# Performance work log

Hardware: AMD Instinct MI355X
Metric: run time of the kernel (lower is better)

## Reference

```python
import jax, jax.numpy as jnp
import numpy as np

DIM = 2048
HEADS = 16
HEAD_DIM = DIM // HEADS  # 128
FF = 8192
MAX_SEQ = 4096
B, S, PREV = 2, 2048, 1024
EPS = 1e-6
ROTARY_BASE = 10000.0


def setup_inputs() -> dict:
    key = jax.random.key(0)
    ks = jax.random.split(key, 16)
    n = lambda k, shape: jax.random.normal(k, shape, jnp.float32) * 0.02
    inp = {
        "x": jax.random.normal(ks[0], (B, S, DIM), jnp.float32),
        "k_cache": jax.random.normal(ks[1], (B, HEADS, PREV, HEAD_DIM), jnp.float32),
        "v_cache": jax.random.normal(ks[2], (B, HEADS, PREV, HEAD_DIM), jnp.float32),
        "attn_norm_w": jnp.ones((DIM,), jnp.float32),
        "ffn_norm_w": jnp.ones((DIM,), jnp.float32),
        "wq": n(ks[3], (DIM, DIM)), "bq": jnp.zeros((DIM,), jnp.float32),
        "wk": n(ks[4], (DIM, DIM)), "bk": jnp.zeros((DIM,), jnp.float32),
        "wv": n(ks[5], (DIM, DIM)), "bv": jnp.zeros((DIM,), jnp.float32),
        "wo": n(ks[6], (DIM, DIM)), "bo": jnp.zeros((DIM,), jnp.float32),
        "w_gate": n(ks[7], (DIM, FF)), "b_gate": jnp.zeros((FF,), jnp.float32),
        "w_val": n(ks[8], (DIM, FF)), "b_val": jnp.zeros((FF,), jnp.float32),
        "w_proj": n(ks[9], (FF, DIM)), "b_proj": jnp.zeros((DIM,), jnp.float32),
    }
    # precompute_freqs_cis as (cos, sin) pair: [MAX_SEQ, HEAD_DIM//2]
    freqs = 1.0 / (ROTARY_BASE ** (np.arange(0, HEAD_DIM, 2)[: HEAD_DIM // 2].astype(np.float32) / HEAD_DIM))
    ang = np.outer(np.arange(MAX_SEQ), freqs).astype(np.float32)
    inp["freqs_cos"] = jnp.asarray(np.cos(ang))
    inp["freqs_sin"] = jnp.asarray(np.sin(ang))
    inp["start_pos"] = PREV
    inp["cache_limit"] = 4096
    return inp


def rmsnorm(x, w):
    return x * jax.lax.rsqrt(jnp.mean(x * x, axis=-1, keepdims=True) + EPS) * w


def rope(x, cos, sin):
    # x: [B, H, S, D]; cos/sin: [1, 1, S, D/2] (complex multiply on even/odd pairs)
    xp = x.reshape(*x.shape[:-1], HEAD_DIM // 2, 2)
    x0, x1 = xp[..., 0], xp[..., 1]
    return jnp.stack([x0 * cos - x1 * sin, x0 * sin + x1 * cos], axis=-1).reshape(x.shape)


def reference(x, k_cache, v_cache, attn_norm_w, ffn_norm_w, wq, bq, wk, bk, wv, bv,
              wo, bo, w_gate, b_gate, w_val, b_val, w_proj, b_proj,
              freqs_cos, freqs_sin, start_pos, cache_limit):
    b, s, d = x.shape
    # --- attention block ---
    h = rmsnorm(x, attn_norm_w)
    split = lambda t: t.reshape(b, s, HEADS, HEAD_DIM).transpose(0, 2, 1, 3)
    q = split(h @ wq + bq)
    k = split(h @ wk + bk)
    v = split(h @ wv + bv)
    pos = (jnp.arange(s) + start_pos) % freqs_cos.shape[0]
    cos = freqs_cos[pos][None, None]  # [1,1,S,D/2]
    sin = freqs_sin[pos][None, None]
    q = rope(q, cos, sin)
    k = rope(k, cos, sin)
    # merge with KV cache (static python slicing for cache_limit)
    k_attn = jnp.concatenate([k_cache, k], axis=2)
    v_attn = jnp.concatenate([v_cache, v], axis=2)
    if cache_limit > 0:
        k_attn = k_attn[:, :, -cache_limit:, :]
        v_attn = v_attn[:, :, -cache_limit:, :]
    t_len = k_attn.shape[2]
    prev = t_len - s
    scores = jnp.einsum('bhsd,bhtd->bhst', q, k_attn) / np.float32(np.sqrt(HEAD_DIM))
    # causal mask: cache fully visible, current block lower-triangular
    allowed = jnp.arange(t_len)[None, :] <= (prev + jnp.arange(s))[:, None]
    scores = jnp.where(allowed, scores, jnp.finfo(scores.dtype).min)
    attn = jax.nn.softmax(scores, axis=-1)
    o = jnp.einsum('bhst,bhtd->bhsd', attn, v_attn).transpose(0, 2, 1, 3).reshape(b, s, d)
    x = x + (o @ wo + bo)
    # --- SwiGLU FFN block ---
    h = rmsnorm(x, ffn_norm_w)
    ff = (jax.nn.silu(h @ w_gate + b_gate) * (h @ w_val + b_val)) @ w_proj + b_proj
    x = x + ff
    return (x, k_attn, v_attn)
```

## Files before the change

### kernel.cpp

```cpp
#include <hip/hip_runtime.h>
#include <stdint.h>

typedef __bf16 bf16x8 __attribute__((ext_vector_type(8)));
typedef float  f32x4  __attribute__((ext_vector_type(4)));

__device__ __forceinline__ uint16_t f2b(float f) {
  uint32_t u = __float_as_uint(f);
  u += 0x7fffu + ((u >> 16) & 1u);
  return (uint16_t)(u >> 16);
}
__device__ __forceinline__ float b2f(uint16_t h) {
  return __uint_as_float(((uint32_t)h) << 16);
}

__device__ __forceinline__ void gl_lds16(const uint16_t* g, uint16_t* l) {
  __builtin_amdgcn_global_load_lds(
      (const __attribute__((address_space(1))) uint32_t*)g,
      (__attribute__((address_space(3))) uint32_t*)l, 16, 0, 0);
}

#define MFMA16(a,b,c) __builtin_amdgcn_mfma_f32_16x16x32_bf16((a),(b),(c),0,0,0)


__global__ __launch_bounds__(256)
void rmsnorm_k(const float* __restrict__ x, const float* __restrict__ w,
               uint16_t* __restrict__ out) {
  __shared__ float red[4];
  const int row = blockIdx.x, tid = threadIdx.x;
  const float* xr = x + (size_t)row * 2048;
  const int c = tid * 8;
  float4 a = *(const float4*)&xr[c];
  float4 b = *(const float4*)&xr[c + 4];
  float ss = a.x*a.x + a.y*a.y + a.z*a.z + a.w*a.w
           + b.x*b.x + b.y*b.y + b.z*b.z + b.w*b.w;
  ss += __shfl_xor(ss, 1);  ss += __shfl_xor(ss, 2);  ss += __shfl_xor(ss, 4);
  ss += __shfl_xor(ss, 8);  ss += __shfl_xor(ss, 16); ss += __shfl_xor(ss, 32);
  if ((tid & 63) == 0) red[tid >> 6] = ss;
  __syncthreads();
  const float tot = red[0] + red[1] + red[2] + red[3];
  const float rms = rsqrtf(tot * (1.0f / 2048.0f) + 1e-6f);
  float4 w0 = *(const float4*)&w[c];
  float4 w1 = *(const float4*)&w[c + 4];
  uint16_t* orow = out + (size_t)row * 2048;
  orow[c+0] = f2b(a.x * rms * w0.x); orow[c+1] = f2b(a.y * rms * w0.y);
  orow[c+2] = f2b(a.z * rms * w0.z); orow[c+3] = f2b(a.w * rms * w0.w);
  orow[c+4] = f2b(b.x * rms * w1.x); orow[c+5] = f2b(b.y * rms * w1.y);
  orow[c+6] = f2b(b.z * rms * w1.z); orow[c+7] = f2b(b.w * rms * w1.w);
}

__global__ void biascat_k(const float* __restrict__ bq, const float* __restrict__ bk,
                          const float* __restrict__ bv, float* __restrict__ out) {
  int i = blockIdx.x * 256 + threadIdx.x;
  if (i < 6144)
    out[i] = (i < 2048) ? bq[i] : ((i < 4096) ? bk[i - 2048] : bv[i - 4096]);
}

__global__ __launch_bounds__(256)
void transpose_k(const float* __restrict__ src, uint16_t* __restrict__ dst,
                 int K, int N) {
  __shared__ float tile[32][33];
  const int tx = threadIdx.x & 31, ty = threadIdx.x >> 5;
  const int n0 = blockIdx.x * 32, k0 = blockIdx.y * 32;
  #pragma unroll
  for (int i = 0; i < 4; ++i)
    tile[ty + i*8][tx] = src[(size_t)(k0 + ty + i*8) * N + n0 + tx];
  __syncthreads();
  #pragma unroll
  for (int i = 0; i < 4; ++i)
    dst[(size_t)(n0 + ty + i*8) * K + k0 + tx] = f2b(tile[tx][ty + i*8]);
}

__global__ __launch_bounds__(256)
void transpose_v_k(const float* __restrict__ src, uint16_t* __restrict__ dst) {
  __shared__ float tile[32][33];
  const int tx = threadIdx.x & 31, ty = threadIdx.x >> 5;
  const int t0 = blockIdx.x * 32, d0 = blockIdx.y * 32, bh = blockIdx.z;
  const float* s = src + (size_t)bh * 393216;
  uint16_t*   d = dst + (size_t)bh * 393216;
  #pragma unroll
  for (int i = 0; i < 4; ++i)
    tile[ty + i*8][tx] = s[(size_t)(t0 + ty + i*8) * 128 + d0 + tx];
  __syncthreads();
  #pragma unroll
  for (int i = 0; i < 4; ++i)
    d[(size_t)(d0 + ty + i*8) * 3072 + t0 + tx] = f2b(tile[tx][ty + i*8]);
}

__global__ __launch_bounds__(256)
void copy_cache_k(const float4* __restrict__ src, float4* __restrict__ dst) {
  const int idx = blockIdx.x * 256 + threadIdx.x;
  const int c4 = idx & 31, t = (idx >> 5) & 1023, bh = idx >> 15;
  dst[((size_t)bh * 3072 + t) * 32 + c4] = src[idx];
}

__global__ __launch_bounds__(256)
void copy_cache_kb_k(const float4* __restrict__ src, float4* __restrict__ dst,
                     uint16_t* __restrict__ dstb) {
  const int idx = blockIdx.x * 256 + threadIdx.x;
  const int c4 = idx & 31, t = (idx >> 5) & 1023, bh = idx >> 15;
  float4 v = src[idx];
  const size_t o = ((size_t)bh * 3072 + t) * 32 + c4;
  dst[o] = v;
  ushort4 b;
  b.x = f2b(v.x); b.y = f2b(v.y); b.z = f2b(v.z); b.w = f2b(v.w);
  ((ushort4*)dstb)[o] = b;
}

__global__ __launch_bounds__(256)
void rope_k(const uint16_t* __restrict__ qkv, const float* __restrict__ fc,
            const float* __restrict__ fs, uint16_t* __restrict__ qb,
            float* __restrict__ kat, float* __restrict__ vat,
            uint16_t* __restrict__ kbb) {
  const int bi = blockIdx.x;
  const int bs = bi >> 2;
  const int h  = ((bi & 3) << 2) + (threadIdx.x >> 6);
  const int d  = threadIdx.x & 63;
  const int b  = bs >> 11, s = bs & 2047;
  const int pos = s + 1024;
  const float c  = fc[pos * 64 + d];
  const float sn = fs[pos * 64 + d];
  const uint16_t* row = qkv + (size_t)bs * 6144 + h * 128;
  const float q0 = b2f(row[2*d]),        q1 = b2f(row[2*d + 1]);
  const float k0 = b2f(row[2048 + 2*d]), k1 = b2f(row[2048 + 2*d + 1]);
  const float v0 = b2f(row[4096 + 2*d]), v1 = b2f(row[4096 + 2*d + 1]);
  const size_t qo = (((size_t)b*16 + h) * 2048 + s) * 128 + 2*d;
  qb[qo]     = f2b(q0 * c - q1 * sn);
  qb[qo + 1] = f2b(q0 * sn + q1 * c);
  const size_t ko = (((size_t)b*16 + h) * 3072 + 1024 + s) * 128 + 2*d;
  const float kr0 = k0 * c - k1 * sn;
  const float kr1 = k0 * sn + k1 * c;
  kat[ko]     = kr0;
  kat[ko + 1] = kr1;
  kbb[ko]     = f2b(kr0);
  kbb[ko + 1] = f2b(kr1);
  vat[ko]     = v0;
  vat[ko + 1] = v1;
}

__global__ __launch_bounds__(256)
void attn_k(const uint16_t* __restrict__ qb, const uint16_t* __restrict__ kb,
            const uint16_t* __restrict__ vt, uint16_t* __restrict__ ob) {
  __shared__ __align__(16) uint16_t lsK[64 * 128];
  __shared__ __align__(16) uint16_t lsV[128 * 64];
  __shared__ __align__(16) uint16_t lsP[4][16 * 72];
  const int tid = threadIdx.x;
  const int lane = tid & 63, w = tid >> 6;
  const int l15 = lane & 15, q4 = lane >> 4;
  const int bh = blockIdx.x & 31;
  const int qi = 31 - (blockIdx.x >> 5);
  const int q0 = qi * 64;
  const int s_w = q0 + w * 16;

  int koff[4], voff[4];
  #pragma unroll
  for (int p = 0; p < 4; ++p) {
    const int idk = p * 256 + tid;
    const int krow = idk >> 4, kch = idk & 15;
    koff[p] = krow * 128 + ((kch ^ (krow & 15)) << 3);
    const int dd = idk >> 3, vch = idk & 7;
    voff[p] = dd * 3072 + ((vch ^ (dd & 7)) << 3);
  }
  const uint16_t* kbh = kb + (size_t)bh * 3072 * 128;
  const uint16_t* vbh = vt + (size_t)bh * 128 * 3072;

  bf16x8 qf[4];
  const uint16_t* qrow = qb + ((size_t)bh * 2048 + s_w + l15) * 128;
  #pragma unroll
  for (int kc = 0; kc < 4; ++kc)
    qf[kc] = *(const bf16x8*)&qrow[kc * 32 + q4 * 8];

  f32x4 o[8];
  #pragma unroll
  for (int nt = 0; nt < 8; ++nt) o[nt] = (f32x4){0.f, 0.f, 0.f, 0.f};
  float mrow[4], lrow[4];
  #pragma unroll
  for (int r = 0; r < 4; ++r) { mrow[r] = -1e38f; lrow[r] = 0.f; }

  const float SC = 0.08838834764831845f * 1.4426950408889634f;
  const int ntiles = qi + 17;
  const int limw = 1024 + s_w + 15;

  for (int tt = 0; tt < ntiles; ++tt) {
    const int t0 = tt << 6;
    __syncthreads();
    #pragma unroll
    for (int p = 0; p < 4; ++p) {
      gl_lds16(kbh + (size_t)t0 * 128 + koff[p], &lsK[(p * 256 + w * 64) * 8]);
      gl_lds16(vbh + t0 + voff[p],               &lsV[(p * 256 + w * 64) * 8]);
    }
    __syncthreads();
    if (t0 > limw) continue;

    f32x4 s[4];
    #pragma unroll
    for (int kg = 0; kg < 4; ++kg) s[kg] = (f32x4){0.f,0.f,0.f,0.f};
    #pragma unroll
    for (int kc = 0; kc < 4; ++kc) {
      const int chp = ((kc * 4 + q4) ^ l15) << 3;
      bf16x8 kf0 = *(const bf16x8*)&lsK[ l15       * 128 + chp];
      bf16x8 kf1 = *(const bf16x8*)&lsK[(16 + l15) * 128 + chp];
      bf16x8 kf2 = *(const bf16x8*)&lsK[(32 + l15) * 128 + chp];
      bf16x8 kf3 = *(const bf16x8*)&lsK[(48 + l15) * 128 + chp];
      s[0] = MFMA16(qf[kc], kf0, s[0]);
      s[1] = MFMA16(qf[kc], kf1, s[1]);
      s[2] = MFMA16(qf[kc], kf2, s[2]);
      s[3] = MFMA16(qf[kc], kf3, s[3]);
    }
    if (t0 + 63 > 1024 + s_w) {
      #pragma unroll
      for (int r = 0; r < 4; ++r) {
        const int lim = 1024 + s_w + q4 * 4 + r;
        if (t0 +      l15 > lim) s[0][r] = -1e38f;
        if (t0 + 16 + l15 > lim) s[1][r] = -1e38f;
        if (t0 + 32 + l15 > lim) s[2][r] = -1e38f;
        if (t0 + 48 + l15 > lim) s[3][r] = -1e38f;
      }
    }
    float alpha[4];
    #pragma unroll
    for (int r = 0; r < 4; ++r) {
      float v = fmaxf(fmaxf(s[0][r], s[1][r]), fmaxf(s[2][r], s[3][r]));
      v = fmaxf(v, __shfl_xor(v, 1)); v = fmaxf(v, __shfl_xor(v, 2));
      v = fmaxf(v, __shfl_xor(v, 4)); v = fmaxf(v, __shfl_xor(v, 8));
      const float mn = fmaxf(mrow[r], v);
      alpha[r] = exp2f((mrow[r] - mn) * SC);
      mrow[r] = mn;
    }
    #pragma unroll
    for (int r = 0; r < 4; ++r) {
      const float nm = -mrow[r] * SC;
      const float p0 = exp2f(fmaf(s[0][r], SC, nm));
      const float p1 = exp2f(fmaf(s[1][r], SC, nm));
      const float p2 = exp2f(fmaf(s[2][r], SC, nm));
      const float p3 = exp2f(fmaf(s[3][r], SC, nm));
      lrow[r] = fmaf(lrow[r], alpha[r], (p0 + p1) + (p2 + p3));
      const int pr = (q4 * 4 + r) * 72;
      lsP[w][pr +      l15] = f2b(p0);
      lsP[w][pr + 16 + l15] = f2b(p1);
      lsP[w][pr + 32 + l15] = f2b(p2);
      lsP[w][pr + 48 + l15] = f2b(p3);
    }
    const float as = alpha[0] * alpha[1] * alpha[2] * alpha[3];
    if (__any(as != 1.0f)) {
      #pragma unroll
      for (int nt = 0; nt < 8; ++nt)
        #pragma unroll
        for (int r = 0; r < 4; ++r) o[nt][r] *= alpha[r];
    }
    bf16x8 pf0 = *(const bf16x8*)&lsP[w][l15 * 72      + q4 * 8];
    bf16x8 pf1 = *(const bf16x8*)&lsP[w][l15 * 72 + 32 + q4 * 8];
    #pragma unroll
    for (int nt = 0; nt < 8; ++nt) {
      const int d = nt * 16 + l15;
      bf16x8 vf0 = *(const bf16x8*)&lsV[d * 64 + (( q4      ^ (d & 7)) << 3)];
      bf16x8 vf1 = *(const bf16x8*)&lsV[d * 64 + (((4 + q4) ^ (d & 7)) << 3)];
      o[nt] = MFMA16(pf0, vf0, o[nt]);
      o[nt] = MFMA16(pf1, vf1, o[nt]);
    }
  }
  const int b = bh >> 4, h = bh & 15;
  #pragma unroll
  for (int r = 0; r < 4; ++r) {
    float l = lrow[r];
    l += __shfl_xor(l, 1); l += __shfl_xor(l, 2);
    l += __shfl_xor(l, 4); l += __shfl_xor(l, 8);
    const float inv = 1.0f / l;
    const int s = s_w + q4 * 4 + r;
    uint16_t* orow = ob + ((size_t)b * 2048 + s) * 2048 + h * 128;
    #pragma unroll
    for (int nt = 0; nt < 8; ++nt)
      orow[nt * 16 + l15] = f2b(o[nt][r] * inv);
  }
}

template <int EPI>
__global__ __launch_bounds__(256)
void gemm_k(const uint16_t* __restrict__ A, const uint16_t* __restrict__ Bt,
            const float* __restrict__ bias, const float* __restrict__ resid,
            const uint16_t* __restrict__ gbuf, void* __restrict__ outp,
            int M, int N, int K) {
  __shared__ __align__(16) uint16_t lsA[128 * 32];
  __shared__ __align__(16) uint16_t lsB[128 * 32];
  const int tid = threadIdx.x;
  const int lane = tid & 63, wvi = tid >> 6;
  const int l15 = lane & 15, q4 = lane >> 4;
  const int wm = wvi & 1, wn = wvi >> 1;
  const int m0 = blockIdx.y * 128, n0 = blockIdx.x * 128;
  const int lr = lane >> 2, lc = (lane & 3) << 3;

  f32x4 acc[4][4];
  #pragma unroll
  for (int i = 0; i < 4; ++i)
    #pragma unroll
    for (int j = 0; j < 4; ++j) acc[i][j] = (f32x4){0.f, 0.f, 0.f, 0.f};

  const uint16_t* Ab = A + (size_t)m0 * K;
  const uint16_t* Bb = Bt + (size_t)n0 * K;
  for (int k0 = 0; k0 < K; k0 += 32) {
    __syncthreads();
    #pragma unroll
    for (int p = 0; p < 2; ++p) {
      const int row = p * 64 + wvi * 16 + lr;
      gl_lds16(Ab + (size_t)row * K + k0 + lc, &lsA[(p * 256 + wvi * 64) * 8]);
      gl_lds16(Bb + (size_t)row * K + k0 + lc, &lsB[(p * 256 + wvi * 64) * 8]);
    }
    __syncthreads();
    bf16x8 af[4], bfr[4];
    #pragma unroll
    for (int i = 0; i < 4; ++i)
      af[i] = *(const bf16x8*)&lsA[(wm * 64 + i * 16 + l15) * 32 + q4 * 8];
    #pragma unroll
    for (int j = 0; j < 4; ++j)
      bfr[j] = *(const bf16x8*)&lsB[(wn * 64 + j * 16 + l15) * 32 + q4 * 8];
    #pragma unroll
    for (int i = 0; i < 4; ++i)
      #pragma unroll
      for (int j = 0; j < 4; ++j)
        acc[i][j] = MFMA16(af[i], bfr[j], acc[i][j]);
  }
  #pragma unroll
  for (int i = 0; i < 4; ++i) {
    #pragma unroll
    for (int j = 0; j < 4; ++j) {
      const int n = n0 + wn * 64 + j * 16 + l15;
      const float bn = bias[n];
      #pragma unroll
      for (int r = 0; r < 4; ++r) {
        const int m = m0 + wm * 64 + i * 16 + q4 * 4 + r;
        const size_t off = (size_t)m * N + n;
        const float v = acc[i][j][r] + bn;
        if (EPI == 0) {
          ((uint16_t*)outp)[off] = f2b(v);
        } else if (EPI == 1) {
          ((float*)outp)[off] = v + resid[off];
        } else {
          const float g = b2f(gbuf[off]);
          const float sg = g / (1.0f + __expf(-g));
          ((uint16_t*)outp)[off] = f2b(sg * v);
        }
      }
    }
  }
}

extern "C" void kernel_launch(void* const* d_in, const int* in_sizes, int n_in,
                              void* d_out, int out_size, void* d_ws, size_t ws_size,
                              hipStream_t stream) {
  const float* x   = (const float*)d_in[0];
  const float* kc  = (const float*)d_in[1];
  const float* vc  = (const float*)d_in[2];
  const float* anw = (const float*)d_in[3];
  const float* fnw = (const float*)d_in[4];
  const float* wq  = (const float*)d_in[5];
  const float* bq  = (const float*)d_in[6];
  const float* wk  = (const float*)d_in[7];
  const float* bk  = (const float*)d_in[8];
  const float* wv_ = (const float*)d_in[9];
  const float* bv  = (const float*)d_in[10];
  const float* wo  = (const float*)d_in[11];
  const float* bo  = (const float*)d_in[12];
  const float* wg  = (const float*)d_in[13];
  const float* bg  = (const float*)d_in[14];
  const float* wva = (const float*)d_in[15];
  const float* bva = (const float*)d_in[16];
  const float* wp  = (const float*)d_in[17];
  const float* bp  = (const float*)d_in[18];
  const float* fc  = (const float*)d_in[19];
  const float* fs  = (const float*)d_in[20];

  float* out_x = (float*)d_out;
  float* kat = out_x + 8388608;
  float* vat = kat + 12582912;

  char* ws = (char*)d_ws;
  uint16_t* h_b   = (uint16_t*)(ws);
  uint16_t* wbuf  = (uint16_t*)(ws + 16777216);
  uint16_t* k_b   = (uint16_t*)(ws);
  uint16_t* v_t   = (uint16_t*)(ws + 25165824);
  uint16_t* qkv_b = (uint16_t*)(ws + 50331648);
  uint16_t* q_b   = (uint16_t*)(ws + 100663296);
  uint16_t* o_b   = (uint16_t*)(ws + 117440512);
  float*    x1    = (float*)   (ws + 134217728);
  float*    bcat  = (float*)   (ws + 167772160);
  uint16_t* g_b   = qkv_b;

  rmsnorm_k<<<4096, 256, 0, stream>>>(x, anw, h_b);
  biascat_k<<<24, 256, 0, stream>>>(bq, bk, bv, bcat);
  transpose_k<<<dim3(64, 64), 256, 0, stream>>>(wq,  wbuf,               2048, 2048);
  transpose_k<<<dim3(64, 64), 256, 0, stream>>>(wk,  wbuf + 1*2048*2048, 2048, 2048);
  transpose_k<<<dim3(64, 64), 256, 0, stream>>>(wv_, wbuf + 2*2048*2048, 2048, 2048);
  gemm_k<0><<<dim3(48, 32), 256, 0, stream>>>(h_b, wbuf, bcat, nullptr, nullptr,
                                              (void*)qkv_b, 4096, 6144, 2048);
  copy_cache_kb_k<<<4096, 256, 0, stream>>>((const float4*)kc, (float4*)kat, k_b);
  copy_cache_k<<<4096, 256, 0, stream>>>((const float4*)vc, (float4*)vat);
  rope_k<<<16384, 256, 0, stream>>>(qkv_b, fc, fs, q_b, kat, vat, k_b);
  transpose_v_k<<<dim3(96, 4, 32), 256, 0, stream>>>(vat, v_t);
  attn_k<<<1024, 256, 0, stream>>>(q_b, k_b, v_t, o_b);
  transpose_k<<<dim3(64, 64), 256, 0, stream>>>(wo, wbuf, 2048, 2048);
  gemm_k<1><<<dim3(16, 32), 256, 0, stream>>>(o_b, wbuf, bo, x, nullptr,
                                              (void*)x1, 4096, 2048, 2048);
  rmsnorm_k<<<4096, 256, 0, stream>>>(x1, fnw, h_b);
  transpose_k<<<dim3(256, 64), 256, 0, stream>>>(wg, wbuf, 2048, 8192);
  gemm_k<0><<<dim3(64, 32), 256, 0, stream>>>(h_b, wbuf, bg, nullptr, nullptr,
                                              (void*)g_b, 4096, 8192, 2048);
  transpose_k<<<dim3(256, 64), 256, 0, stream>>>(wva, wbuf, 2048, 8192);
  gemm_k<2><<<dim3(64, 32), 256, 0, stream>>>(h_b, wbuf, bva, nullptr, g_b,
                                              (void*)g_b, 4096, 8192, 2048);
  transpose_k<<<dim3(64, 256), 256, 0, stream>>>(wp, wbuf, 8192, 2048);
  gemm_k<1><<<dim3(16, 32), 256, 0, stream>>>(g_b, wbuf, bp, x1, nullptr,
                                              (void*)out_x, 4096, 2048, 8192);
}
```

Before: 1.384 ms.

## Replace GEMM with 256-wide double-buffered, swizzled, XCD-remapped tile kernel

Replaces the 128x128 single-buffered GEMM with a templated kernel that uses 128x256 or 256x256 output tiles and 512 threads. LDS tiles are filled with global_load_lds into an XOR-swizzled, double-buffered layout, so the next K-slab loads while MFMAs run on the current one. Workgroup IDs are remapped so that neighbouring tiles land on the same XCD, and s_setprio raises wave priority during MFMA bursts. The kernel needs up to 128KB of dynamic LDS, which cuts occupancy to about one block per CU. It also relies on hand-tuned vmcnt waits that are only correct for these load counts.

```diff
diff --git a/kernel.cpp b/kernel.cpp
--- a/kernel.cpp
+++ b/kernel.cpp
@@ -273,62 +273,129 @@
   }
 }
 
-template <int EPI>
-__global__ __launch_bounds__(256)
-void gemm_k(const uint16_t* __restrict__ A, const uint16_t* __restrict__ Bt,
-            const float* __restrict__ bias, const float* __restrict__ resid,
-            const uint16_t* __restrict__ gbuf, void* __restrict__ outp,
-            int M, int N, int K) {
-  __shared__ __align__(16) uint16_t lsA[128 * 32];
-  __shared__ __align__(16) uint16_t lsB[128 * 32];
+template <int MR, int EPI>
+__global__ __launch_bounds__(512, 2)
+void gemm256_k(const uint16_t* __restrict__ A, const uint16_t* __restrict__ Bt,
+               const float* __restrict__ bias, const float* __restrict__ resid,
+               const uint16_t* __restrict__ gbuf, void* __restrict__ outp,
+               int M, int N, int K) {
+  constexpr int BM = MR * 32;
+  constexpr int AL = BM / 128;
+  extern __shared__ __align__(16) uint16_t dynls[];
+  uint16_t* lsA = dynls;
+  uint16_t* lsB = dynls + 4 * BM * 32;
+
   const int tid = threadIdx.x;
-  const int lane = tid & 63, wvi = tid >> 6;
+  const int lane = tid & 63, w = tid >> 6;
   const int l15 = lane & 15, q4 = lane >> 4;
-  const int wm = wvi & 1, wn = wvi >> 1;
-  const int m0 = blockIdx.y * 128, n0 = blockIdx.x * 128;
-  const int lr = lane >> 2, lc = (lane & 3) << 3;
-
-  f32x4 acc[4][4];
-  #pragma unroll
-  for (int i = 0; i < 4; ++i)
-    #pragma unroll
-    for (int j = 0; j < 4; ++j) acc[i][j] = (f32x4){0.f, 0.f, 0.f, 0.f};
-
+  const int wm = w & 1, wn = w >> 1;
+
+  const int nwg = gridDim.x * gridDim.y;
+  const int orig = blockIdx.y * gridDim.x + blockIdx.x;
+  const int qq = nwg >> 3, rr = nwg & 7;
+  const int xcd = orig & 7, loc = orig >> 3;
+  const int wgid = (xcd < rr ? xcd * (qq + 1) : rr * (qq + 1) + (xcd - rr) * qq) + loc;
+  const int n0 = (wgid % gridDim.x) * 256;
+  const int m0 = (wgid / gridDim.x) * BM;
+
+  int arow[AL], acsl[AL];
+  #pragma unroll
+  for (int j = 0; j < AL; ++j) {
+    const int g = (w * AL + j) * 64 + lane;
+    arow[j] = g >> 2;
+    acsl[j] = (((g & 3) ^ ((g >> 3) & 3)) << 3);
+  }
+  int brow[2], bcsl[2];
+  #pragma unroll
+  for (int j = 0; j < 2; ++j) {
+    const int g = (w * 2 + j) * 64 + lane;
+    brow[j] = g >> 2;
+    bcsl[j] = (((g & 3) ^ ((g >> 3) & 3)) << 3);
+  }
   const uint16_t* Ab = A + (size_t)m0 * K;
   const uint16_t* Bb = Bt + (size_t)n0 * K;
-  for (int k0 = 0; k0 < K; k0 += 32) {
-    __syncthreads();
-    #pragma unroll
-    for (int p = 0; p < 2; ++p) {
-      const int row = p * 64 + wvi * 16 + lr;
-      gl_lds16(Ab + (size_t)row * K + k0 + lc, &lsA[(p * 256 + wvi * 64) * 8]);
-      gl_lds16(Bb + (size_t)row * K + k0 + lc, &lsB[(p * 256 + wvi * 64) * 8]);
-    }
-    __syncthreads();
-    bf16x8 af[4], bfr[4];
-    #pragma unroll
-    for (int i = 0; i < 4; ++i)
-      af[i] = *(const bf16x8*)&lsA[(wm * 64 + i * 16 + l15) * 32 + q4 * 8];
-    #pragma unroll
-    for (int j = 0; j < 4; ++j)
-      bfr[j] = *(const bf16x8*)&lsB[(wn * 64 + j * 16 + l15) * 32 + q4 * 8];
-    #pragma unroll
-    for (int i = 0; i < 4; ++i)
+
+  f32x4 acc[MR][4];
+  #pragma unroll
+  for (int m = 0; m < MR; ++m)
+    #pragma unroll
+    for (int n = 0; n < 4; ++n) acc[m][n] = (f32x4){0.f, 0.f, 0.f, 0.f};
+
+  auto STAGE = [&](int kt, int b, int kk) {
+    const int kbase = kt * 64 + kk * 32;
+    #pragma unroll
+    for (int j = 0; j < AL; ++j)
+      gl_lds16(Ab + (size_t)arow[j] * K + kbase + acsl[j],
+               lsA + (b * 2 + kk) * (BM * 32) + (w * AL + j) * 512);
+    #pragma unroll
+    for (int j = 0; j < 2; ++j)
+      gl_lds16(Bb + (size_t)brow[j] * K + kbase + bcsl[j],
+               lsB + (b * 2 + kk) * 8192 + (w * 2 + j) * 512);
+  };
+  auto COMPUTE = [&](int b, int kk) {
+    bf16x8 af[MR], bfr[4];
+    #pragma unroll
+    for (int m = 0; m < MR; ++m) {
+      const int row = wm * (BM / 2) + m * 16 + l15;
+      af[m] = *(const bf16x8*)(lsA + ((b * 2 + kk) * BM + row) * 32 +
+                               ((q4 ^ ((row >> 1) & 3)) << 3));
+    }
+    #pragma unroll
+    for (int n = 0; n < 4; ++n) {
+      const int row = wn * 64 + n * 16 + l15;
+      bfr[n] = *(const bf16x8*)(lsB + (b * 2 + kk) * 8192 + row * 32 +
+                                ((q4 ^ ((row >> 1) & 3)) << 3));
+    }
+    __builtin_amdgcn_s_setprio(1);
+    #pragma unroll
+    for (int m = 0; m < MR; ++m)
       #pragma unroll
-      for (int j = 0; j < 4; ++j)
-        acc[i][j] = MFMA16(af[i], bfr[j], acc[i][j]);
-  }
-  #pragma unroll
-  for (int i = 0; i < 4; ++i) {
-    #pragma unroll
-    for (int j = 0; j < 4; ++j) {
-      const int n = n0 + wn * 64 + j * 16 + l15;
-      const float bn = bias[n];
+      for (int n = 0; n < 4; ++n)
+        acc[m][n] = MFMA16(af[m], bfr[n], acc[m][n]);
+    __builtin_amdgcn_s_setprio(0);
+  };
+  auto WAITP = [&](bool pf) {
+    if (pf) {
+      if constexpr (AL == 2) asm volatile("s_waitcnt vmcnt(4)" ::: "memory");
+      else                   asm volatile("s_waitcnt vmcnt(3)" ::: "memory");
+    } else {
+      asm volatile("s_waitcnt vmcnt(0)" ::: "memory");
+    }
+  };
+
+  const int nK = K >> 6;
+  STAGE(0, 0, 0);
+  STAGE(0, 0, 1);
+  WAITP(true);
+  __builtin_amdgcn_s_barrier();
+  asm volatile("" ::: "memory");
+
+  for (int t = 0; t < nK; ++t) {
+    const int b = t & 1;
+    const bool pf = (t + 1 < nK);
+    if (pf) STAGE(t + 1, b ^ 1, 0);
+    COMPUTE(b, 0);
+    WAITP(pf);
+    __builtin_amdgcn_s_barrier();
+    asm volatile("" ::: "memory");
+    if (pf) STAGE(t + 1, b ^ 1, 1);
+    COMPUTE(b, 1);
+    WAITP(pf);
+    __builtin_amdgcn_s_barrier();
+    asm volatile("" ::: "memory");
+  }
+
+  #pragma unroll
+  for (int m = 0; m < MR; ++m) {
+    #pragma unroll
+    for (int n = 0; n < 4; ++n) {
+      const int nn = n0 + wn * 64 + n * 16 + l15;
+      const float bn = bias[nn];
       #pragma unroll
       for (int r = 0; r < 4; ++r) {
-        const int m = m0 + wm * 64 + i * 16 + q4 * 4 + r;
-        const size_t off = (size_t)m * N + n;
-        const float v = acc[i][j][r] + bn;
+        const int mm = m0 + wm * (BM / 2) + m * 16 + q4 * 4 + r;
+        const size_t off = (size_t)mm * N + nn;
+        const float v = acc[m][n][r] + bn;
         if (EPI == 0) {
           ((uint16_t*)outp)[off] = f2b(v);
         } else if (EPI == 1) {
@@ -384,29 +451,42 @@
   float*    bcat  = (float*)   (ws + 167772160);
   uint16_t* g_b   = qkv_b;
 
+  {
+    auto f40 = gemm256_k<4, 0>; auto f41 = gemm256_k<4, 1>;
+    auto f80 = gemm256_k<8, 0>; auto f82 = gemm256_k<8, 2>;
+    (void)hipFuncSetAttribute((const void*)f40,
+        hipFuncAttributeMaxDynamicSharedMemorySize, 98304);
+    (void)hipFuncSetAttribute((const void*)f41,
+        hipFuncAttributeMaxDynamicSharedMemorySize, 98304);
+    (void)hipFuncSetAttribute((const void*)f80,
+        hipFuncAttributeMaxDynamicSharedMemorySize, 131072);
+    (void)hipFuncSetAttribute((const void*)f82,
+        hipFuncAttributeMaxDynamicSharedMemorySize, 131072);
+  }
+
   rmsnorm_k<<<4096, 256, 0, stream>>>(x, anw, h_b);
   biascat_k<<<24, 256, 0, stream>>>(bq, bk, bv, bcat);
   transpose_k<<<dim3(64, 64), 256, 0, stream>>>(wq,  wbuf,               2048, 2048);
   transpose_k<<<dim3(64, 64), 256, 0, stream>>>(wk,  wbuf + 1*2048*2048, 2048, 2048);
   transpose_k<<<dim3(64, 64), 256, 0, stream>>>(wv_, wbuf + 2*2048*2048, 2048, 2048);
-  gemm_k<0><<<dim3(48, 32), 256, 0, stream>>>(h_b, wbuf, bcat, nullptr, nullptr,
-                                              (void*)qkv_b, 4096, 6144, 2048);
+  gemm256_k<4,0><<<dim3(24, 32), 512, 98304, stream>>>(h_b, wbuf, bcat, nullptr,
+                                              nullptr, (void*)qkv_b, 4096, 6144, 2048);
   copy_cache_kb_k<<<4096, 256, 0, stream>>>((const float4*)kc, (float4*)kat, k_b);
   copy_cache_k<<<4096, 256, 0, stream>>>((const float4*)vc, (float4*)vat);
   rope_k<<<16384, 256, 0, stream>>>(qkv_b, fc, fs, q_b, kat, vat, k_b);
   transpose_v_k<<<dim3(96, 4, 32), 256, 0, stream>>>(vat, v_t);
   attn_k<<<1024, 256, 0, stream>>>(q_b, k_b, v_t, o_b);
   transpose_k<<<dim3(64, 64), 256, 0, stream>>>(wo, wbuf, 2048, 2048);
-  gemm_k<1><<<dim3(16, 32), 256, 0, stream>>>(o_b, wbuf, bo, x, nullptr,
+  gemm256_k<4,1><<<dim3(8, 32), 512, 98304, stream>>>(o_b, wbuf, bo, x, nullptr,
                                               (void*)x1, 4096, 2048, 2048);
   rmsnorm_k<<<4096, 256, 0, stream>>>(x1, fnw, h_b);
   transpose_k<<<dim3(256, 64), 256, 0, stream>>>(wg, wbuf, 2048, 8192);
-  gemm_k<0><<<dim3(64, 32), 256, 0, stream>>>(h_b, wbuf, bg, nullptr, nullptr,
-                                              (void*)g_b, 4096, 8192, 2048);
+  gemm256_k<8,0><<<dim3(32, 16), 512, 131072, stream>>>(h_b, wbuf, bg, nullptr,
+                                              nullptr, (void*)g_b, 4096, 8192, 2048);
   transpose_k<<<dim3(256, 64), 256, 0, stream>>>(wva, wbuf, 2048, 8192);
-  gemm_k<2><<<dim3(64, 32), 256, 0, stream>>>(h_b, wbuf, bva, nullptr, g_b,
-                                              (void*)g_b, 4096, 8192, 2048);
+  gemm256_k<8,2><<<dim3(32, 16), 512, 131072, stream>>>(h_b, wbuf, bva, nullptr,
+                                              g_b, (void*)g_b, 4096, 8192, 2048);
   transpose_k<<<dim3(64, 256), 256, 0, stream>>>(wp, wbuf, 8192, 2048);
-  gemm_k<1><<<dim3(16, 32), 256, 0, stream>>>(g_b, wbuf, bp, x1, nullptr,
+  gemm256_k<4,1><<<dim3(8, 32), 512, 98304, stream>>>(g_b, wbuf, bp, x1, nullptr,
                                               (void*)out_x, 4096, 2048, 8192);
 }
```

Measured after the change: 1.254 ms. -9.4%, faster.
